# Performance work log

Hardware: AMD Instinct MI355X
Metric: run time of the kernel (lower is better)

The kernel has to match this reference:

```python
import jax, jax.numpy as jnp
import numpy as np

N = 100000
NNZ = 1600000
C_IN = 128
C_OUT = 128


def setup_inputs() -> dict:
    key = jax.random.key(0)
    ks = jax.random.split(key, 9)
    phi_indices = jax.random.randint(ks[0], (2, NNZ), 0, N, dtype=jnp.int64)
    phi_values = jax.random.uniform(ks[1], (NNZ,), dtype=jnp.float32)
    phi_inverse_indices = jax.random.randint(ks[2], (2, NNZ), 0, N, dtype=jnp.int64)
    phi_inverse_values = jax.random.uniform(ks[3], (NNZ,), dtype=jnp.float32)
    # feature matrix is N x C_IN sparse: row in [0,N), col in [0,C_IN)
    f_rows = jax.random.randint(ks[4], (NNZ,), 0, N, dtype=jnp.int64)
    f_cols = jax.random.randint(ks[5], (NNZ,), 0, C_IN, dtype=jnp.int64)
    feature_indices = jnp.stack([f_rows, f_cols], axis=0)
    feature_values = jax.random.uniform(ks[6], (NNZ,), dtype=jnp.float32)
    # xavier-uniform weight, diagonal filter ~ U(0.9, 1.1)
    limit = float(np.sqrt(6.0 / (C_IN + C_OUT)))
    weight_matrix = jax.random.uniform(ks[7], (C_IN, C_OUT), minval=-limit, maxval=limit, dtype=jnp.float32)
    diagonal_weight_filter = jax.random.uniform(ks[8], (N, 1), minval=0.9, maxval=1.1, dtype=jnp.float32)
    return {
        "phi_indices": phi_indices,
        "phi_values": phi_values,
        "phi_inverse_indices": phi_inverse_indices,
        "phi_inverse_values": phi_inverse_values,
        "feature_indices": feature_indices,
        "feature_values": feature_values,
        "weight_matrix": weight_matrix,
        "diagonal_weight_filter": diagonal_weight_filter,
        "dropout": 0,
    }


def _spmm(indices, values, dense, n_rows):
    # sparse (n_rows x K) @ dense (K x C): gather dense rows by col index,
    # scale by values, scatter-add into output rows.
    rows, cols = indices[0], indices[1]
    contrib = values[:, None] * dense[cols]  # [nnz, C]
    return jax.ops.segment_sum(contrib, rows, num_segments=n_rows)


def reference(phi_indices, phi_values, phi_inverse_indices, phi_inverse_values,
              feature_indices, feature_values, weight_matrix,
              diagonal_weight_filter, dropout):
    n = diagonal_weight_filter.shape[0]
    # filtered = F_sparse @ W   -> [N, C_out]
    filtered = _spmm(feature_indices, feature_values, weight_matrix, n)
    # Phi @ diag(theta) @ Phi_inv @ filtered, computed right-to-left:
    z = _spmm(phi_inverse_indices, phi_inverse_values, filtered, n)  # Phi_inv @ filtered
    z = diagonal_weight_filter * z  # row-rescale by diagonal Theta
    localized = _spmm(phi_indices, phi_values, z, n)  # Phi @ (...)
    # F.dropout with training=False is identity; relu only
    return jax.nn.relu(localized)
```

## Files before the change

kernel.cpp:

```cpp
#include <hip/hip_runtime.h>

#define CH 128
#define SUMS_BLOCK 512
#define CHUNK_E 4096
#define RPT 16
#define BUCKET_BITS 10
#define BKEYS (1 << BUCKET_BITS)
#define NBMAX 512
#define STAG_CAP 18432

__device__ inline ushort f2bf(float f) {
    unsigned b = __float_as_uint(f);
    return (ushort)((b + 0x7FFF + ((b >> 16) & 1)) >> 16);
}
__device__ inline float bf2f(ushort u) {
    return __uint_as_float((unsigned)u << 16);
}

__global__ void conv_w_kernel(const float* __restrict__ W,
                              ushort* __restrict__ Wb) {
    int i = blockIdx.x * blockDim.x + threadIdx.x;
    if (i < CH * CH) Wb[i] = f2bf(W[i]);
}

__global__ __launch_bounds__(256) void passA_sort(const int* __restrict__ idxA,
                                                  const float* __restrict__ valA,
                                                  const int* __restrict__ idxB,
                                                  const float* __restrict__ valB,
                                                  const int* __restrict__ idxC,
                                                  const float* __restrict__ valC,
                                                  const float* __restrict__ theta,
                                                  int nnz, int n, int nb,
                                                  int* __restrict__ locA,
                                                  int2* __restrict__ recsTmp) {
    __shared__ int hist[NBMAX];
    __shared__ int sc[NBMAX];
    __shared__ int cur[NBMAX];
    int t = threadIdx.x;
    hist[t] = 0; hist[t + 256] = 0;
    __syncthreads();

    int base = blockIdx.x * CHUNK_E;
    int end = min(base + CHUNK_E, 3 * nnz);
    int csize = end - base;
    int rbeg = base + t * RPT;

    int px[RPT];
    int pv[RPT];
    short pb[RPT];

    int nvalid = 0;
    if (rbeg + RPT <= nnz) {
        #pragma unroll
        for (int r4 = 0; r4 < RPT / 4; ++r4) {
            int4 k4 = *reinterpret_cast<const int4*>(&idxA[rbeg + r4 * 4]);
            int4 c4 = *reinterpret_cast<const int4*>(&idxA[nnz + rbeg + r4 * 4]);
            float4 v4 = *reinterpret_cast<const float4*>(&valA[rbeg + r4 * 4]);
            int kk[4] = {k4.x, k4.y, k4.z, k4.w};
            int cc[4] = {c4.x, c4.y, c4.z, c4.w};
            float vv[4] = {v4.x, v4.y, v4.z, v4.w};
            #pragma unroll
            for (int u = 0; u < 4; ++u) {
                int r = r4 * 4 + u;
                px[r] = cc[u] | ((kk[u] & (BKEYS - 1)) << 17);
                pv[r] = __float_as_int(vv[u]);
                pb[r] = (short)(kk[u] >> BUCKET_BITS);
                atomicAdd(&hist[pb[r]], 1);
            }
        }
        nvalid = RPT;
    } else if (rbeg >= nnz && rbeg + RPT <= 2 * nnz) {
        int e0 = rbeg - nnz;
        #pragma unroll
        for (int r4 = 0; r4 < RPT / 4; ++r4) {
            int4 k4 = *reinterpret_cast<const int4*>(&idxB[e0 + r4 * 4]);
            int4 c4 = *reinterpret_cast<const int4*>(&idxB[nnz + e0 + r4 * 4]);
            float4 v4 = *reinterpret_cast<const float4*>(&valB[e0 + r4 * 4]);
            int kk[4] = {k4.x, k4.y, k4.z, k4.w};
            int cc[4] = {c4.x, c4.y, c4.z, c4.w};
            float vv[4] = {v4.x, v4.y, v4.z, v4.w};
            #pragma unroll
            for (int u = 0; u < 4; ++u) {
                int r = r4 * 4 + u;
                int key = n + kk[u];
                px[r] = cc[u] | ((key & (BKEYS - 1)) << 17);
                pv[r] = __float_as_int(vv[u] * theta[cc[u]]);
                pb[r] = (short)(key >> BUCKET_BITS);
                atomicAdd(&hist[pb[r]], 1);
            }
        }
        nvalid = RPT;
    } else if (rbeg >= 2 * nnz && rbeg + RPT <= 3 * nnz) {
        int e0 = rbeg - 2 * nnz;
        #pragma unroll
        for (int r4 = 0; r4 < RPT / 4; ++r4) {
            int4 k4 = *reinterpret_cast<const int4*>(&idxC[e0 + r4 * 4]);
            int4 c4 = *reinterpret_cast<const int4*>(&idxC[nnz + e0 + r4 * 4]);
            float4 v4 = *reinterpret_cast<const float4*>(&valC[e0 + r4 * 4]);
            int kk[4] = {k4.x, k4.y, k4.z, k4.w};
            int cc[4] = {c4.x, c4.y, c4.z, c4.w};
            float vv[4] = {v4.x, v4.y, v4.z, v4.w};
            #pragma unroll
            for (int u = 0; u < 4; ++u) {
                int r = r4 * 4 + u;
                int key = 2 * n + kk[u];
                px[r] = cc[u] | ((key & (BKEYS - 1)) << 17);
                pv[r] = __float_as_int(vv[u]);
                pb[r] = (short)(key >> BUCKET_BITS);
                atomicAdd(&hist[pb[r]], 1);
            }
        }
        nvalid = RPT;
    } else {
        #pragma unroll
        for (int r = 0; r < RPT; ++r) {
            int i = rbeg + r;
            if (i >= end) break;
            int key, c;
            float v;
            if (i < nnz) {
                key = idxA[i];
                c = idxA[nnz + i];
                v = valA[i];
            } else if (i < 2 * nnz) {
                int e = i - nnz;
                key = n + idxB[e];
                c = idxB[nnz + e];
                v = valB[e] * theta[c];
            } else {
                int e = i - 2 * nnz;
                key = 2 * n + idxC[e];
                c = idxC[nnz + e];
                v = valC[e];
            }
            px[r] = c | ((key & (BKEYS - 1)) << 17);
            pv[r] = __float_as_int(v);
            pb[r] = (short)(key >> BUCKET_BITS);
            atomicAdd(&hist[pb[r]], 1);
            ++nvalid;
        }
    }
    __syncthreads();

    sc[t] = hist[t]; sc[t + 256] = hist[t + 256];
    __syncthreads();
    for (int off = 1; off < NBMAX; off <<= 1) {
        int a = (t >= off) ? sc[t - off] : 0;
        int b2 = (t + 256 >= off) ? sc[t + 256 - off] : 0;
        __syncthreads();
        sc[t] += a; sc[t + 256] += b2;
        __syncthreads();
    }
    cur[t] = sc[t] - hist[t];
    cur[t + 256] = sc[t + 256] - hist[t + 256];
    __syncthreads();

    for (int b = t; b <= nb; b += 256)
        locA[(size_t)blockIdx.x * (nb + 1) + b] = (b < nb) ? (sc[b] - hist[b]) : csize;

    #pragma unroll
    for (int r = 0; r < RPT; ++r) {
        if (r < nvalid) {
            int pos = atomicAdd(&cur[pb[r]], 1);
            recsTmp[(size_t)base + pos] = make_int2(px[r], pv[r]);
        }
    }
}

__global__ __launch_bounds__(256) void bucket_totals(const int* __restrict__ locA,
                                                     int nchA, int nb,
                                                     int* __restrict__ tot) {
    __shared__ int red[256];
    int b = blockIdx.x;
    int t = threadIdx.x;
    int s = 0;
    for (int ch = t; ch < nchA; ch += 256) {
        const int* lc = &locA[(size_t)ch * (nb + 1)];
        s += lc[b + 1] - lc[b];
    }
    red[t] = s;
    __syncthreads();
    for (int off = 128; off > 0; off >>= 1) {
        if (t < off) red[t] += red[t + off];
        __syncthreads();
    }
    if (t == 0) tot[b] = red[0];
}

__global__ void scan_sums_kernel(int* __restrict__ chunk_sums, int nchunks) {
    __shared__ int tmp[SUMS_BLOCK];
    __shared__ int carry_s;
    int tid = threadIdx.x;
    if (tid == 0) carry_s = 0;
    __syncthreads();
    for (int base = 0; base < nchunks; base += SUMS_BLOCK) {
        int i = base + tid;
        int v = (i < nchunks) ? chunk_sums[i] : 0;
        tmp[tid] = v;
        __syncthreads();
        for (int off = 1; off < SUMS_BLOCK; off <<= 1) {
            int y = (tid >= off) ? tmp[tid - off] : 0;
            __syncthreads();
            tmp[tid] += y;
            __syncthreads();
        }
        int c = carry_s;
        if (i < nchunks) chunk_sums[i] = tmp[tid] - v + c;
        int total = tmp[SUMS_BLOCK - 1];
        __syncthreads();
        if (tid == 0) carry_s = c + total;
        __syncthreads();
    }
}

__global__ __launch_bounds__(1024) void passB_kernel(const int2* __restrict__ recsTmp,
                                                     const int* __restrict__ locA,
                                                     const int* __restrict__ bsArr,
                                                     int nchA, int nb, int n3,
                                                     int* __restrict__ start_g,
                                                     int* __restrict__ counts_g,
                                                     unsigned* __restrict__ recs) {
    __shared__ int hist[BKEYS];
    __shared__ int scan[BKEYS];
    __shared__ unsigned outb[STAG_CAP];
    int b = blockIdx.x;
    int t = threadIdx.x;
    int wave = t >> 6, lane = t & 63;
    int grp = lane >> 4, gl = lane & 15;
    int bs = bsArr[b];
    hist[t] = 0;
    __syncthreads();

    for (int ch = wave * 4 + grp; ch < nchA; ch += 64) {
        const int* lc = &locA[(size_t)ch * (nb + 1)];
        int ls = lc[b], le = lc[b + 1];
        size_t cb = (size_t)ch * CHUNK_E;
        for (int k = ls + gl; k < le; k += 16)
            atomicAdd(&hist[(recsTmp[cb + k].x >> 17) & (BKEYS - 1)], 1);
    }
    __syncthreads();

    int v = hist[t];
    scan[t] = v;
    __syncthreads();
    for (int off = 1; off < BKEYS; off <<= 1) {
        int y = (t >= off) ? scan[t - off] : 0;
        __syncthreads();
        scan[t] += y;
        __syncthreads();
    }
    int excl = scan[t] - v;
    int key = (b << BUCKET_BITS) + t;
    if (key < n3) {
        start_g[key] = bs + excl;
        counts_g[key] = v;
    }
    int totalB = scan[BKEYS - 1];
    hist[t] = excl;
    __syncthreads();

    if (totalB <= STAG_CAP) {
        for (int ch = wave * 4 + grp; ch < nchA; ch += 64) {
            const int* lc = &locA[(size_t)ch * (nb + 1)];
            int ls = lc[b], le = lc[b + 1];
            size_t cb = (size_t)ch * CHUNK_E;
            for (int k = ls + gl; k < le; k += 16) {
                int2 r = recsTmp[cb + k];
                int kk = (r.x >> 17) & (BKEYS - 1);
                int pos = atomicAdd(&hist[kk], 1);
                unsigned c = (unsigned)(r.x & 0x1FFFF);
                unsigned bv = (unsigned)f2bf(__int_as_float(r.y)) & 0x7FFFu;
                outb[pos] = (c << 15) | bv;
            }
        }
        __syncthreads();
        for (int k = t; k < totalB; k += 1024)
            recs[(size_t)bs + k] = outb[k];
    } else {
        for (int ch = wave * 4 + grp; ch < nchA; ch += 64) {
            const int* lc = &locA[(size_t)ch * (nb + 1)];
            int ls = lc[b], le = lc[b + 1];
            size_t cb = (size_t)ch * CHUNK_E;
            for (int k = ls + gl; k < le; k += 16) {
                int2 r = recsTmp[cb + k];
                int kk = (r.x >> 17) & (BKEYS - 1);
                int pos = atomicAdd(&hist[kk], 1);
                unsigned c = (unsigned)(r.x & 0x1FFFF);
                unsigned bv = (unsigned)f2bf(__int_as_float(r.y)) & 0x7FFFu;
                recs[(size_t)bs + pos] = (c << 15) | bv;
            }
        }
    }
}

__global__ __launch_bounds__(256) void pull_spmm_bf16(
        const unsigned* __restrict__ recs,
        const int* __restrict__ start,
        const int* __restrict__ counts,
        const ushort* __restrict__ dense,
        ushort* __restrict__ outb,
        float* __restrict__ outf,
        int n, int do_relu) {
    int wave = threadIdx.x >> 6;
    int lane = threadIdx.x & 63;
    int row = blockIdx.x * 4 + wave;
    if (row >= n) return;
    int s = start[row];
    int cnt = counts[row];
    const ushort2* dp = reinterpret_cast<const ushort2*>(dense);
    float ax = 0.0f, ay = 0.0f;
    int j = 0;
    for (; j + 4 <= cnt; j += 4) {
        unsigned r0 = recs[s + j + 0];
        unsigned r1 = recs[s + j + 1];
        unsigned r2 = recs[s + j + 2];
        unsigned r3 = recs[s + j + 3];
        ushort2 d0 = dp[(size_t)(r0 >> 15) * 64 + lane];
        ushort2 d1 = dp[(size_t)(r1 >> 15) * 64 + lane];
        ushort2 d2 = dp[(size_t)(r2 >> 15) * 64 + lane];
        ushort2 d3 = dp[(size_t)(r3 >> 15) * 64 + lane];
        float v0 = __uint_as_float((r0 & 0x7FFFu) << 16);
        float v1 = __uint_as_float((r1 & 0x7FFFu) << 16);
        float v2 = __uint_as_float((r2 & 0x7FFFu) << 16);
        float v3 = __uint_as_float((r3 & 0x7FFFu) << 16);
        ax = fmaf(v0, bf2f(d0.x), ax); ay = fmaf(v0, bf2f(d0.y), ay);
        ax = fmaf(v1, bf2f(d1.x), ax); ay = fmaf(v1, bf2f(d1.y), ay);
        ax = fmaf(v2, bf2f(d2.x), ax); ay = fmaf(v2, bf2f(d2.y), ay);
        ax = fmaf(v3, bf2f(d3.x), ax); ay = fmaf(v3, bf2f(d3.y), ay);
    }
    for (; j < cnt; ++j) {
        unsigned r0 = recs[s + j];
        ushort2 d0 = dp[(size_t)(r0 >> 15) * 64 + lane];
        float v0 = __uint_as_float((r0 & 0x7FFFu) << 16);
        ax = fmaf(v0, bf2f(d0.x), ax); ay = fmaf(v0, bf2f(d0.y), ay);
    }
    if (do_relu) { ax = fmaxf(ax, 0.0f); ay = fmaxf(ay, 0.0f); }
    if (outb) {
        ushort2 o = {f2bf(ax), f2bf(ay)};
        reinterpret_cast<ushort2*>(outb)[(size_t)row * 64 + lane] = o;
    } else {
        float2 o = {ax, ay};
        *reinterpret_cast<float2*>(&outf[(size_t)row * CH + lane * 2]) = o;
    }
}


extern "C" void kernel_launch(void* const* d_in, const int* in_sizes, int n_in,
                              void* d_out, int out_size, void* d_ws, size_t ws_size,
                              hipStream_t stream) {
    const int*   phi_idx  = (const int*)d_in[0];
    const float* phi_val  = (const float*)d_in[1];
    const int*   phii_idx = (const int*)d_in[2];
    const float* phii_val = (const float*)d_in[3];
    const int*   f_idx    = (const int*)d_in[4];
    const float* f_val    = (const float*)d_in[5];
    const float* W        = (const float*)d_in[6];
    const float* theta    = (const float*)d_in[7];

    const int nnz = in_sizes[1];
    const int n   = in_sizes[7];
    const int n3  = 3 * n;
    const int total = 3 * nnz;

    const int nb   = (n3 + BKEYS - 1) >> BUCKET_BITS;
    const int nchA = (total + CHUNK_E - 1) / CHUNK_E;

    float* out = (float*)d_out;

    char* ws = (char*)d_ws;
    char*  dense_region = ws;
    int2*  recsTmp  = (int2*)dense_region;
    ushort* filt_b  = (ushort*)dense_region;
    ushort* z_b     = (ushort*)(dense_region + (size_t)n * CH * sizeof(ushort));
    ws += (size_t)n * CH * sizeof(float);
    unsigned* recs  = (unsigned*)ws;        ws += (size_t)total * sizeof(unsigned);
    int* counts     = (int*)ws;             ws += (size_t)n3 * sizeof(int);
    int* start      = (int*)ws;             ws += (size_t)n3 * sizeof(int);
    int* locA       = (int*)ws;             ws += (size_t)nchA * (nb + 1) * sizeof(int);
    int* tot        = (int*)ws;             ws += 4096;
    ushort* w_b     = (ushort*)ws;          ws += CH * CH * sizeof(ushort);

    const int row_blocks = (n + 3) / 4;

    conv_w_kernel<<<(CH * CH + 255) / 256, 256, 0, stream>>>(W, w_b);

    passA_sort<<<nchA, 256, 0, stream>>>(phii_idx, phii_val, phi_idx, phi_val,
                                         f_idx, f_val, theta,
                                         nnz, n, nb, locA, recsTmp);
    bucket_totals<<<nb, 256, 0, stream>>>(locA, nchA, nb, tot);
    scan_sums_kernel<<<1, SUMS_BLOCK, 0, stream>>>(tot, nb);
    passB_kernel<<<nb, 1024, 0, stream>>>(recsTmp, locA, tot, nchA, nb, n3,
                                          start, counts, recs);

    pull_spmm_bf16<<<row_blocks, 256, 0, stream>>>(
        recs, start + 2 * n, counts + 2 * n, w_b, filt_b, nullptr, n, 0);

    pull_spmm_bf16<<<row_blocks, 256, 0, stream>>>(
        recs, start, counts, filt_b, z_b, nullptr, n, 0);

    pull_spmm_bf16<<<row_blocks, 256, 0, stream>>>(
        recs, start + n, counts + n, z_b, nullptr, out, n, 1);
}
```

Measured before the change: 272.4 us.

## Use half-wave per row with 8-byte gathers and shuffled record broadcast

The pull SpMM now assigns 32 lanes per output row instead of a full 64-lane wave, so each lane loads four bf16 values (ushort4) per gathered row and a block covers 8 rows. Edge records are loaded cooperatively, one per lane in batches of 32, and broadcast with __shfl rather than every lane reading each record redundantly. The goal is fewer, wider memory transactions, less redundant record traffic and more rows in flight per wave. The cost is the shuffle overhead and two rows with different edge counts sharing one wave, which can cause divergence.

```diff
diff --git a/kernel.cpp b/kernel.cpp
--- a/kernel.cpp
+++ b/kernel.cpp
@@ -301,46 +301,59 @@
         ushort* __restrict__ outb,
         float* __restrict__ outf,
         int n, int do_relu) {
-    int wave = threadIdx.x >> 6;
-    int lane = threadIdx.x & 63;
-    int row = blockIdx.x * 4 + wave;
+    int grp32 = threadIdx.x >> 5;
+    int lane = threadIdx.x & 31;
+    int row = blockIdx.x * 8 + grp32;
     if (row >= n) return;
     int s = start[row];
     int cnt = counts[row];
-    const ushort2* dp = reinterpret_cast<const ushort2*>(dense);
-    float ax = 0.0f, ay = 0.0f;
-    int j = 0;
-    for (; j + 4 <= cnt; j += 4) {
-        unsigned r0 = recs[s + j + 0];
-        unsigned r1 = recs[s + j + 1];
-        unsigned r2 = recs[s + j + 2];
-        unsigned r3 = recs[s + j + 3];
-        ushort2 d0 = dp[(size_t)(r0 >> 15) * 64 + lane];
-        ushort2 d1 = dp[(size_t)(r1 >> 15) * 64 + lane];
-        ushort2 d2 = dp[(size_t)(r2 >> 15) * 64 + lane];
-        ushort2 d3 = dp[(size_t)(r3 >> 15) * 64 + lane];
-        float v0 = __uint_as_float((r0 & 0x7FFFu) << 16);
-        float v1 = __uint_as_float((r1 & 0x7FFFu) << 16);
-        float v2 = __uint_as_float((r2 & 0x7FFFu) << 16);
-        float v3 = __uint_as_float((r3 & 0x7FFFu) << 16);
-        ax = fmaf(v0, bf2f(d0.x), ax); ay = fmaf(v0, bf2f(d0.y), ay);
-        ax = fmaf(v1, bf2f(d1.x), ax); ay = fmaf(v1, bf2f(d1.y), ay);
-        ax = fmaf(v2, bf2f(d2.x), ax); ay = fmaf(v2, bf2f(d2.y), ay);
-        ax = fmaf(v3, bf2f(d3.x), ax); ay = fmaf(v3, bf2f(d3.y), ay);
-    }
-    for (; j < cnt; ++j) {
-        unsigned r0 = recs[s + j];
-        ushort2 d0 = dp[(size_t)(r0 >> 15) * 64 + lane];
-        float v0 = __uint_as_float((r0 & 0x7FFFu) << 16);
-        ax = fmaf(v0, bf2f(d0.x), ax); ay = fmaf(v0, bf2f(d0.y), ay);
-    }
-    if (do_relu) { ax = fmaxf(ax, 0.0f); ay = fmaxf(ay, 0.0f); }
+    const ushort4* dp = reinterpret_cast<const ushort4*>(dense);
+    float a0 = 0.0f, a1 = 0.0f, a2 = 0.0f, a3 = 0.0f;
+
+    for (int jb = 0; jb < cnt; jb += 32) {
+        int nbatch = min(32, cnt - jb);
+        unsigned myrec = (lane < nbatch) ? recs[s + jb + lane] : 0u;
+        int j = 0;
+        for (; j + 4 <= nbatch; j += 4) {
+            unsigned r0 = __shfl(myrec, j + 0, 32);
+            unsigned r1 = __shfl(myrec, j + 1, 32);
+            unsigned r2 = __shfl(myrec, j + 2, 32);
+            unsigned r3 = __shfl(myrec, j + 3, 32);
+            ushort4 d0 = dp[(size_t)(r0 >> 15) * 32 + lane];
+            ushort4 d1 = dp[(size_t)(r1 >> 15) * 32 + lane];
+            ushort4 d2 = dp[(size_t)(r2 >> 15) * 32 + lane];
+            ushort4 d3 = dp[(size_t)(r3 >> 15) * 32 + lane];
+            float v0 = __uint_as_float((r0 & 0x7FFFu) << 16);
+            float v1 = __uint_as_float((r1 & 0x7FFFu) << 16);
+            float v2 = __uint_as_float((r2 & 0x7FFFu) << 16);
+            float v3 = __uint_as_float((r3 & 0x7FFFu) << 16);
+            a0 = fmaf(v0, bf2f(d0.x), a0); a1 = fmaf(v0, bf2f(d0.y), a1);
+            a2 = fmaf(v0, bf2f(d0.z), a2); a3 = fmaf(v0, bf2f(d0.w), a3);
+            a0 = fmaf(v1, bf2f(d1.x), a0); a1 = fmaf(v1, bf2f(d1.y), a1);
+            a2 = fmaf(v1, bf2f(d1.z), a2); a3 = fmaf(v1, bf2f(d1.w), a3);
+            a0 = fmaf(v2, bf2f(d2.x), a0); a1 = fmaf(v2, bf2f(d2.y), a1);
+            a2 = fmaf(v2, bf2f(d2.z), a2); a3 = fmaf(v2, bf2f(d2.w), a3);
+            a0 = fmaf(v3, bf2f(d3.x), a0); a1 = fmaf(v3, bf2f(d3.y), a1);
+            a2 = fmaf(v3, bf2f(d3.z), a2); a3 = fmaf(v3, bf2f(d3.w), a3);
+        }
+        for (; j < nbatch; ++j) {
+            unsigned r0 = __shfl(myrec, j, 32);
+            ushort4 d0 = dp[(size_t)(r0 >> 15) * 32 + lane];
+            float v0 = __uint_as_float((r0 & 0x7FFFu) << 16);
+            a0 = fmaf(v0, bf2f(d0.x), a0); a1 = fmaf(v0, bf2f(d0.y), a1);
+            a2 = fmaf(v0, bf2f(d0.z), a2); a3 = fmaf(v0, bf2f(d0.w), a3);
+        }
+    }
+    if (do_relu) {
+        a0 = fmaxf(a0, 0.0f); a1 = fmaxf(a1, 0.0f);
+        a2 = fmaxf(a2, 0.0f); a3 = fmaxf(a3, 0.0f);
+    }
     if (outb) {
-        ushort2 o = {f2bf(ax), f2bf(ay)};
-        reinterpret_cast<ushort2*>(outb)[(size_t)row * 64 + lane] = o;
+        ushort4 o = {f2bf(a0), f2bf(a1), f2bf(a2), f2bf(a3)};
+        reinterpret_cast<ushort4*>(outb)[(size_t)row * 32 + lane] = o;
     } else {
-        float2 o = {ax, ay};
-        *reinterpret_cast<float2*>(&outf[(size_t)row * CH + lane * 2]) = o;
+        float4 o = {a0, a1, a2, a3};
+        *reinterpret_cast<float4*>(&outf[(size_t)row * CH + lane * 4]) = o;
     }
 }
 
@@ -380,7 +393,7 @@
     int* tot        = (int*)ws;             ws += 4096;
     ushort* w_b     = (ushort*)ws;          ws += CH * CH * sizeof(ushort);
 
-    const int row_blocks = (n + 3) / 4;
+    const int row_blocks = (n + 7) / 8;
 
     conv_w_kernel<<<(CH * CH + 255) / 256, 256, 0, stream>>>(W, w_b);
 
```

Result: faster. 236.6 us (median of 2 runs) (-13.2%).
